# Kernel tuning notes

Hardware: AMD Instinct MI355X
Metric: run time of the kernel (lower is better)

Reference implementation:

```python
import jax, jax.numpy as jnp
import numpy as np

NEG_INF = jnp.float32(-1e9)  # finite large-negative avoids -inf*0 NaNs in grads


def setup_inputs() -> dict:
    key = jax.random.key(0)
    k1, k2, k3, k4, k5 = jax.random.split(key, 5)
    B, T, S, D = 16, 1024, 2048, 1024
    source = jax.random.normal(k1, (B, T, D), dtype=jnp.float32)
    memory_bank = jax.random.normal(k2, (B, S, D), dtype=jnp.float32)
    memory_lengths = jax.random.randint(k3, (B,), 1, S + 1, dtype=jnp.int32)
    # torch nn.Linear weights are [out_features, in_features]
    W_in = jax.random.normal(k4, (D, D), dtype=jnp.float32) / jnp.sqrt(jnp.float32(D))
    W_out = jax.random.normal(k5, (D, 2 * D), dtype=jnp.float32) / jnp.sqrt(jnp.float32(2 * D))
    return {"source": source, "memory_bank": memory_bank,
            "memory_lengths": memory_lengths, "W_in": W_in, "W_out": W_out}


def reference(source, memory_bank, memory_lengths, W_in, W_out):
    # GlobalAttention(attn_type='general', attn_func='softmax'), multi-step path
    B, T, D = source.shape
    S = memory_bank.shape[1]
    # score: general -> linear_in(h_t) @ h_s^T
    h_t = jnp.einsum('btd,ed->bte', source, W_in)            # [B,T,D]
    align = jnp.einsum('bte,bse->bts', h_t, memory_bank)      # [B,T,S]
    # sequence_mask on memory_lengths, broadcast over target dim
    mask = jnp.arange(S, dtype=jnp.int32)[None, None, :] < memory_lengths[:, None, None]
    align = jnp.where(mask, align, NEG_INF)
    align_vectors = jax.nn.softmax(align, axis=-1)            # [B,T,S]
    c = jnp.einsum('bts,bsd->btd', align_vectors, memory_bank)  # [B,T,D]
    concat_c = jnp.concatenate([c, source], axis=-1)          # [B,T,2D]
    attn_h = jnp.einsum('btf,of->bto', concat_c, W_out)       # linear_out, no bias for 'general'
    attn_h = jnp.tanh(attn_h)
    # not one_step -> transpose to [T,B,*]
    return attn_h.transpose(1, 0, 2), align_vectors.transpose(1, 0, 2)
```

## Files before the change

kernel.cpp:

```cpp
#include <hip/hip_runtime.h>

typedef __attribute__((ext_vector_type(8))) short s16x8;
typedef __attribute__((ext_vector_type(4))) float f32x4;
typedef __attribute__((ext_vector_type(4))) unsigned short u16x4;
typedef unsigned short u16;

__device__ __forceinline__ u16 f2bf(float x) {
  unsigned u = __builtin_bit_cast(unsigned, x);
  u = u + 0x7fffu + ((u >> 16) & 1u);
  return (u16)(u >> 16);
}
__device__ __forceinline__ float bf2f(u16 h) {
  return __builtin_bit_cast(float, (unsigned)h << 16);
}
__device__ __forceinline__ void split_bf(float x, u16 &h, u16 &l) {
  h = f2bf(x); l = f2bf(x - bf2f(h));
}

typedef __attribute__((address_space(1))) const unsigned int as1c_u32;
typedef __attribute__((address_space(3))) unsigned int as3_u32;
__device__ __forceinline__ void gload16(const void* g, void* l) {
  __builtin_amdgcn_global_load_lds((as1c_u32*)g, (as3_u32*)l, 16, 0, 0);
}

__global__ __launch_bounds__(256) void split_copy_k(
    const float* __restrict__ in, u16* __restrict__ oh, u16* __restrict__ ol, long n4) {
  const long i = (long)blockIdx.x * 256 + threadIdx.x;
  if (i >= n4) return;
  const f32x4 v = *(const f32x4*)(in + i * 4);
  u16x4 h, l;
#pragma unroll
  for (int e = 0; e < 4; ++e) { u16 hh, ll; split_bf(v[e], hh, ll); h[e] = hh; l[e] = ll; }
  *(u16x4*)(oh + i * 4) = h;
  *(u16x4*)(ol + i * 4) = l;
}

__global__ __launch_bounds__(256) void split_hi_k(
    const float* __restrict__ in, u16* __restrict__ oh, long n4) {
  const long i = (long)blockIdx.x * 256 + threadIdx.x;
  if (i >= n4) return;
  const f32x4 v = *(const f32x4*)(in + i * 4);
  u16x4 h;
#pragma unroll
  for (int e = 0; e < 4; ++e) h[e] = f2bf(v[e]);
  *(u16x4*)(oh + i * 4) = h;
}

__global__ __launch_bounds__(256) void transpose_bf_k(
    const u16* __restrict__ in, u16* __restrict__ outT) {
  __shared__ u16 tile[64][72];
  const int b = blockIdx.z;
  const int s0 = blockIdx.x * 64, d0 = blockIdx.y * 64;
  const u16* pin = in + (long)b * 2048 * 1024;
  u16* pout = outT + (long)b * 1024 * 2048;
  const int t = threadIdx.x;
#pragma unroll
  for (int i = 0; i < 4; ++i) {
    const int idx = i * 256 + t;
    const int r = idx >> 4;
    const int c4 = (idx & 15) * 4;
    *(u16x4*)&tile[r][c4] = *(const u16x4*)&pin[(long)(s0 + r) * 1024 + d0 + c4];
  }
  __syncthreads();
#pragma unroll
  for (int i = 0; i < 4; ++i) {
    const int idx = i * 256 + t;
    const int r = idx >> 4;
    const int c4 = (idx & 15) * 4;
    u16x4 v = { tile[c4][r], tile[c4 + 1][r], tile[c4 + 2][r], tile[c4 + 3][r] };
    *(u16x4*)&pout[(long)(d0 + r) * 2048 + s0 + c4] = v;
  }
}

__global__ __launch_bounds__(256) void softmax_k(
    float* __restrict__ alignBuf, const int* __restrict__ lens, float* __restrict__ outP) {
  const int row = blockIdx.x;
  const int b = row >> 10;
  const int tt = row & 1023;
  const int len = lens[b];
  float* arow = alignBuf + (long)row * 2048;
  const int t = threadIdx.x;
  const int lane = t & 63, wv = t >> 6;
  float v[8];
  float mx = -3.0e38f;
#pragma unroll
  for (int j = 0; j < 8; ++j) {
    const int s = j * 256 + t;
    float x = arow[s];
    x = (s < len) ? x : -1.0e9f;
    v[j] = x;
    mx = fmaxf(mx, x);
  }
#pragma unroll
  for (int off = 32; off; off >>= 1) mx = fmaxf(mx, __shfl_xor(mx, off));
  __shared__ float redm[4], reds[4];
  if (lane == 0) redm[wv] = mx;
  __syncthreads();
  mx = fmaxf(fmaxf(redm[0], redm[1]), fmaxf(redm[2], redm[3]));
  float e[8]; float sum = 0.f;
#pragma unroll
  for (int j = 0; j < 8; ++j) { e[j] = __expf(v[j] - mx); sum += e[j]; }
#pragma unroll
  for (int off = 32; off; off >>= 1) sum += __shfl_xor(sum, off);
  if (lane == 0) reds[wv] = sum;
  __syncthreads();
  sum = reds[0] + reds[1] + reds[2] + reds[3];
  const float inv = 1.0f / sum;
  u16* ph = (u16*)arow;
  u16* pl = ph + 2048;
  float* orow = outP + ((long)tt * 16 + b) * 2048;
#pragma unroll
  for (int j = 0; j < 8; ++j) {
    const int s = j * 256 + t;
    const float pv = e[j] * inv;
    orow[s] = pv;
    u16 h, l; split_bf(pv, h, l);
    ph[s] = h; pl[s] = l;
  }
}

template<int NPROD, int EP, int MASK>
__global__ __launch_bounds__(512, 2) void gemm256(
    const u16* __restrict__ Ah, const u16* __restrict__ Al,
    const u16* __restrict__ Ah2, const u16* __restrict__ Al2,
    int kSplitA, int lda, long sA,
    const u16* __restrict__ Bh, const u16* __restrict__ Bl, int ldb, long sB,
    int K, const int* __restrict__ lens,
    float* __restrict__ Cf, u16* __restrict__ Ch, u16* __restrict__ Cl,
    int ldc, long sC, int lgx, int lgxy, int nwg) {
  constexpr int NT = (NPROD >= 3) ? 4 : (NPROD == 2 ? 3 : 2);
  __shared__ __align__(16) u16 lds0[NT][8192];
  __shared__ __align__(16) u16 lds1[NT][8192];

  const int orig = blockIdx.x;
  const int wg = (orig & 7) * (nwg >> 3) + (orig >> 3);
  const int bx = wg & ((1 << lgx) - 1);
  const int by = (wg >> lgx) & ((1 << (lgxy - lgx)) - 1);
  const int bz = wg >> lgxy;

  const long m0 = (long)by * 256;
  const long n0 = (long)bx * 256;

  int Klim = K;
  if constexpr (MASK == 1) {
    const int len = lens[bz];
    if (n0 >= len) return;
  } else if constexpr (MASK == 2) {
    const int len = lens[bz];
    const int kl = (len + 31) & ~31;
    Klim = kl < K ? kl : K;
  }

  const u16* pAh  = Ah  + (long)bz * sA;
  const u16* pAl  = Al  + (long)bz * sA;
  const u16* pAh2 = Ah2 + (long)bz * sA;
  const u16* pAl2 = Al2 + (long)bz * sA;
  const u16* pBh  = Bh  + (long)bz * sB;
  const u16* pBl  = Bl  + (long)bz * sB;

  const int t = threadIdx.x;
  const int lane = t & 63;
  const int wv = t >> 6;
  const int wm = wv >> 2;
  const int wn = wv & 3;
  const int lk = lane >> 4;
  const int lr = lane & 15;

  f32x4 acc[8][4];
#pragma unroll
  for (int i = 0; i < 8; ++i)
#pragma unroll
    for (int j = 0; j < 4; ++j) acc[i][j] = 0.0f;

  auto stage = [&](u16 (*L)[8192], int k0) {
#pragma unroll
    for (int j = 0; j < 2; ++j) {
      const int ci = (j * 8 + wv) * 64;
      const int c = ci + lane;
      const int kc = c >> 8;
      const int r = c & 255;
      const int k = k0 + kc * 8;
      const u16 *aH = pAh, *aL = pAl;
      long ka = k;
      if (k >= kSplitA) { aH = pAh2; aL = pAl2; ka = k - kSplitA; }
      const long aoff = (m0 + r) * (long)lda + ka;
      gload16(aH + aoff, &L[0][ci * 8]);
      if constexpr (NPROD >= 2) gload16(aL + aoff, &L[2][ci * 8]);
      const long boff = (n0 + r) * (long)ldb + k;
      gload16(pBh + boff, &L[1][ci * 8]);
      if constexpr (NPROD >= 3) gload16(pBl + boff, &L[3][ci * 8]);
    }
  };

  auto compute = [&](u16 (*L)[8192]) {
    s16x8 bh[4], bl[4];
#pragma unroll
    for (int fn = 0; fn < 4; ++fn) {
      const int rb = wn * 64 + fn * 16 + lr;
      bh[fn] = *(const s16x8*)&L[1][lk * 2048 + rb * 8];
      if constexpr (NPROD >= 3) bl[fn] = *(const s16x8*)&L[3][lk * 2048 + rb * 8];
    }
#pragma unroll
    for (int fm = 0; fm < 8; ++fm) {
      const int ra = wm * 128 + fm * 16 + lr;
      const s16x8 ah = *(const s16x8*)&L[0][lk * 2048 + ra * 8];
      s16x8 al;
      if constexpr (NPROD >= 2) al = *(const s16x8*)&L[2][lk * 2048 + ra * 8];
#pragma unroll
      for (int fn = 0; fn < 4; ++fn) {
        acc[fm][fn] = __builtin_amdgcn_mfma_f32_16x16x32_bf16(ah, bh[fn], acc[fm][fn], 0, 0, 0);
        if constexpr (NPROD >= 3)
          acc[fm][fn] = __builtin_amdgcn_mfma_f32_16x16x32_bf16(ah, bl[fn], acc[fm][fn], 0, 0, 0);
        if constexpr (NPROD >= 2)
          acc[fm][fn] = __builtin_amdgcn_mfma_f32_16x16x32_bf16(al, bh[fn], acc[fm][fn], 0, 0, 0);
      }
    }
  };

  const int KT = Klim >> 5;
  stage(lds0, 0);
  __syncthreads();
  for (int kt = 0; kt < KT; kt += 2) {
    if (kt + 1 < KT) stage(lds1, (kt + 1) << 5);
    compute(lds0);
    __syncthreads();
    if (kt + 1 < KT) {
      if (kt + 2 < KT) stage(lds0, (kt + 2) << 5);
      compute(lds1);
      __syncthreads();
    }
  }

#pragma unroll
  for (int fm = 0; fm < 8; ++fm)
#pragma unroll
    for (int fn = 0; fn < 4; ++fn)
#pragma unroll
      for (int r = 0; r < 4; ++r) {
        const long row = m0 + wm * 128 + fm * 16 + (lane >> 4) * 4 + r;
        const long col = n0 + wn * 64 + fn * 16 + lr;
        const float v = acc[fm][fn][r];
        if constexpr (EP == 0) {
          Cf[(long)bz * sC + row * ldc + col] = v;
        } else if constexpr (EP == 1) {
          u16 h, l; split_bf(v, h, l);
          const long o = (long)bz * sC + row * ldc + col;
          Ch[o] = h; Cl[o] = l;
        } else {
          const long bb = row >> 10;
          const long tt = row & 1023;
          Cf[(tt * 16 + bb) * (long)ldc + col] = tanhf(v);
        }
      }
}

extern "C" void kernel_launch(void* const* d_in, const int* in_sizes, int n_in,
                              void* d_out, int out_size, void* d_ws, size_t ws_size,
                              hipStream_t stream) {
  (void)in_sizes; (void)n_in; (void)out_size; (void)ws_size;
  const float* src = (const float*)d_in[0];
  const float* mb  = (const float*)d_in[1];
  const int*   lens= (const int*)d_in[2];
  const float* Wi  = (const float*)d_in[3];
  const float* Wo  = (const float*)d_in[4];
  float* out = (float*)d_out;

  char* p = (char*)d_ws;
  u16* mbS_hi  = (u16*)p;
  u16* mbS_lo  = (u16*)(p + (64L << 20));
  u16* srcU_hi = (u16*)(p + (128L << 20));
  u16* srcU_lo = (u16*)(p + (160L << 20));
  u16* htc_hi  = (u16*)(p + (192L << 20));
  u16* htc_lo  = (u16*)(p + (224L << 20));
  float* alignBuf = (float*)(p + (256L << 20));
  u16* Wi_hi = (u16*)alignBuf;
  u16* Wi_lo = Wi_hi + 1048576;
  u16* mbT   = mbS_lo;
  u16* Wo_hi = mbS_hi;

  dim3 blk(256);
  split_copy_k<<<dim3(32768), blk, 0, stream>>>(mb,  mbS_hi, mbS_lo, 8388608L);
  split_copy_k<<<dim3(16384), blk, 0, stream>>>(src, srcU_hi, srcU_lo, 4194304L);
  split_copy_k<<<dim3(1024),  blk, 0, stream>>>(Wi,  Wi_hi,  Wi_lo,  262144L);

  gemm256<3, 1, 0><<<dim3(256), dim3(512), 0, stream>>>(
      srcU_hi, srcU_lo, srcU_hi, srcU_lo, 1 << 30, 1024, 0L,
      Wi_hi, Wi_lo, 1024, 0L,
      1024, lens,
      nullptr, htc_hi, htc_lo, 1024, 0L,
      2, 8, 256);

  gemm256<3, 0, 1><<<dim3(512), dim3(512), 0, stream>>>(
      htc_hi, htc_lo, htc_hi, htc_lo, 1 << 30, 1024, 1048576L,
      mbS_hi, mbS_lo, 1024, 2097152L,
      1024, lens,
      alignBuf, nullptr, nullptr, 2048, 2097152L,
      3, 5, 512);

  softmax_k<<<dim3(16384), blk, 0, stream>>>(alignBuf, lens, out + 16777216L);

  transpose_bf_k<<<dim3(32, 16, 16), blk, 0, stream>>>(mbS_hi, mbT);
  split_hi_k<<<dim3(2048), blk, 0, stream>>>(Wo, Wo_hi, 524288L);

  gemm256<2, 1, 2><<<dim3(256), dim3(512), 0, stream>>>(
      (const u16*)alignBuf, (const u16*)alignBuf + 2048,
      (const u16*)alignBuf, (const u16*)alignBuf + 2048, 1 << 30, 4096, 4194304L,
      mbT, mbT, 2048, 2097152L,
      2048, lens,
      nullptr, htc_hi, htc_lo, 1024, 1048576L,
      2, 4, 256);

  gemm256<2, 2, 0><<<dim3(256), dim3(512), 0, stream>>>(
      htc_hi, htc_lo, srcU_hi, srcU_lo, 1024, 1024, 0L,
      Wo_hi, Wo_hi, 2048, 0L,
      2048, lens,
      out, nullptr, nullptr, 1024, 0L,
      2, 8, 256);
}
```

Before: 975.7 us.

## Shrink GEMM tiles to 128x128 with 256 threads and single-buffered LDS

Replaces the 256x256-tile, 512-thread double-buffered GEMM with a 128x128-tile, 256-thread kernel that uses one LDS buffer and syncs twice per K step. Launch grids grow fourfold to cover the same outputs. The goal is more workgroups and occupancy across the CUs. In exchange it gives up operand reuse per tile and the overlap of global loads with MFMA compute that double buffering provided.

```diff
diff --git a/kernel.cpp b/kernel.cpp
--- a/kernel.cpp
+++ b/kernel.cpp
@@ -120,7 +120,7 @@
 }
 
 template<int NPROD, int EP, int MASK>
-__global__ __launch_bounds__(512, 2) void gemm256(
+__global__ __launch_bounds__(256) void gemm128(
     const u16* __restrict__ Ah, const u16* __restrict__ Al,
     const u16* __restrict__ Ah2, const u16* __restrict__ Al2,
     int kSplitA, int lda, long sA,
@@ -129,8 +129,7 @@
     float* __restrict__ Cf, u16* __restrict__ Ch, u16* __restrict__ Cl,
     int ldc, long sC, int lgx, int lgxy, int nwg) {
   constexpr int NT = (NPROD >= 3) ? 4 : (NPROD == 2 ? 3 : 2);
-  __shared__ __align__(16) u16 lds0[NT][8192];
-  __shared__ __align__(16) u16 lds1[NT][8192];
+  __shared__ __align__(16) u16 lds[NT][4096];
 
   const int orig = blockIdx.x;
   const int wg = (orig & 7) * (nwg >> 3) + (orig >> 3);
@@ -138,16 +137,14 @@
   const int by = (wg >> lgx) & ((1 << (lgxy - lgx)) - 1);
   const int bz = wg >> lgxy;
 
-  const long m0 = (long)by * 256;
-  const long n0 = (long)bx * 256;
+  const long m0 = (long)by * 128;
+  const long n0 = (long)bx * 128;
 
   int Klim = K;
   if constexpr (MASK == 1) {
-    const int len = lens[bz];
-    if (n0 >= len) return;
+    if (n0 >= lens[bz]) return;
   } else if constexpr (MASK == 2) {
-    const int len = lens[bz];
-    const int kl = (len + 31) & ~31;
+    const int kl = (lens[bz] + 31) & ~31;
     Klim = kl < K ? kl : K;
   }
 
@@ -161,83 +158,67 @@
   const int t = threadIdx.x;
   const int lane = t & 63;
   const int wv = t >> 6;
-  const int wm = wv >> 2;
-  const int wn = wv & 3;
+  const int wm = wv >> 1;
+  const int wn = wv & 1;
   const int lk = lane >> 4;
   const int lr = lane & 15;
 
-  f32x4 acc[8][4];
-#pragma unroll
-  for (int i = 0; i < 8; ++i)
+  f32x4 acc[4][4];
+#pragma unroll
+  for (int i = 0; i < 4; ++i)
 #pragma unroll
     for (int j = 0; j < 4; ++j) acc[i][j] = 0.0f;
 
-  auto stage = [&](u16 (*L)[8192], int k0) {
+  for (int k0 = 0; k0 < Klim; k0 += 32) {
+    __syncthreads();
 #pragma unroll
     for (int j = 0; j < 2; ++j) {
-      const int ci = (j * 8 + wv) * 64;
+      const int ci = (j * 4 + wv) * 64;
       const int c = ci + lane;
-      const int kc = c >> 8;
-      const int r = c & 255;
+      const int kc = c >> 7;
+      const int r = c & 127;
       const int k = k0 + kc * 8;
       const u16 *aH = pAh, *aL = pAl;
       long ka = k;
       if (k >= kSplitA) { aH = pAh2; aL = pAl2; ka = k - kSplitA; }
       const long aoff = (m0 + r) * (long)lda + ka;
-      gload16(aH + aoff, &L[0][ci * 8]);
-      if constexpr (NPROD >= 2) gload16(aL + aoff, &L[2][ci * 8]);
+      gload16(aH + aoff, &lds[0][ci * 8]);
+      if constexpr (NPROD >= 2) gload16(aL + aoff, &lds[2][ci * 8]);
       const long boff = (n0 + r) * (long)ldb + k;
-      gload16(pBh + boff, &L[1][ci * 8]);
-      if constexpr (NPROD >= 3) gload16(pBl + boff, &L[3][ci * 8]);
+      gload16(pBh + boff, &lds[1][ci * 8]);
+      if constexpr (NPROD >= 3) gload16(pBl + boff, &lds[3][ci * 8]);
     }
-  };
-
-  auto compute = [&](u16 (*L)[8192]) {
-    s16x8 bh[4], bl[4];
-#pragma unroll
-    for (int fn = 0; fn < 4; ++fn) {
-      const int rb = wn * 64 + fn * 16 + lr;
-      bh[fn] = *(const s16x8*)&L[1][lk * 2048 + rb * 8];
-      if constexpr (NPROD >= 3) bl[fn] = *(const s16x8*)&L[3][lk * 2048 + rb * 8];
+    __syncthreads();
+
+    s16x8 ah[4], al[4], bh[4], bl[4];
+#pragma unroll
+    for (int f = 0; f < 4; ++f) {
+      const int ra = wm * 64 + f * 16 + lr;
+      const int rb = wn * 64 + f * 16 + lr;
+      ah[f] = *(const s16x8*)&lds[0][lk * 1024 + ra * 8];
+      bh[f] = *(const s16x8*)&lds[1][lk * 1024 + rb * 8];
+      if constexpr (NPROD >= 2) al[f] = *(const s16x8*)&lds[2][lk * 1024 + ra * 8];
+      if constexpr (NPROD >= 3) bl[f] = *(const s16x8*)&lds[3][lk * 1024 + rb * 8];
     }
 #pragma unroll
-    for (int fm = 0; fm < 8; ++fm) {
-      const int ra = wm * 128 + fm * 16 + lr;
-      const s16x8 ah = *(const s16x8*)&L[0][lk * 2048 + ra * 8];
-      s16x8 al;
-      if constexpr (NPROD >= 2) al = *(const s16x8*)&L[2][lk * 2048 + ra * 8];
-#pragma unroll
-      for (int fn = 0; fn < 4; ++fn) {
-        acc[fm][fn] = __builtin_amdgcn_mfma_f32_16x16x32_bf16(ah, bh[fn], acc[fm][fn], 0, 0, 0);
+    for (int i = 0; i < 4; ++i)
+#pragma unroll
+      for (int j = 0; j < 4; ++j) {
+        acc[i][j] = __builtin_amdgcn_mfma_f32_16x16x32_bf16(ah[i], bh[j], acc[i][j], 0, 0, 0);
         if constexpr (NPROD >= 3)
-          acc[fm][fn] = __builtin_amdgcn_mfma_f32_16x16x32_bf16(ah, bl[fn], acc[fm][fn], 0, 0, 0);
+          acc[i][j] = __builtin_amdgcn_mfma_f32_16x16x32_bf16(ah[i], bl[j], acc[i][j], 0, 0, 0);
         if constexpr (NPROD >= 2)
-          acc[fm][fn] = __builtin_amdgcn_mfma_f32_16x16x32_bf16(al, bh[fn], acc[fm][fn], 0, 0, 0);
+          acc[i][j] = __builtin_amdgcn_mfma_f32_16x16x32_bf16(al[i], bh[j], acc[i][j], 0, 0, 0);
       }
-    }
-  };
-
-  const int KT = Klim >> 5;
-  stage(lds0, 0);
-  __syncthreads();
-  for (int kt = 0; kt < KT; kt += 2) {
-    if (kt + 1 < KT) stage(lds1, (kt + 1) << 5);
-    compute(lds0);
-    __syncthreads();
-    if (kt + 1 < KT) {
-      if (kt + 2 < KT) stage(lds0, (kt + 2) << 5);
-      compute(lds1);
-      __syncthreads();
-    }
-  }
-
-#pragma unroll
-  for (int fm = 0; fm < 8; ++fm)
+  }
+
+#pragma unroll
+  for (int fm = 0; fm < 4; ++fm)
 #pragma unroll
     for (int fn = 0; fn < 4; ++fn)
 #pragma unroll
       for (int r = 0; r < 4; ++r) {
-        const long row = m0 + wm * 128 + fm * 16 + (lane >> 4) * 4 + r;
+        const long row = m0 + wm * 64 + fm * 16 + (lane >> 4) * 4 + r;
         const long col = n0 + wn * 64 + fn * 16 + lr;
         const float v = acc[fm][fn][r];
         if constexpr (EP == 0) {
@@ -283,37 +264,37 @@
   split_copy_k<<<dim3(16384), blk, 0, stream>>>(src, srcU_hi, srcU_lo, 4194304L);
   split_copy_k<<<dim3(1024),  blk, 0, stream>>>(Wi,  Wi_hi,  Wi_lo,  262144L);
 
-  gemm256<3, 1, 0><<<dim3(256), dim3(512), 0, stream>>>(
+  gemm128<3, 1, 0><<<dim3(1024), blk, 0, stream>>>(
       srcU_hi, srcU_lo, srcU_hi, srcU_lo, 1 << 30, 1024, 0L,
       Wi_hi, Wi_lo, 1024, 0L,
       1024, lens,
       nullptr, htc_hi, htc_lo, 1024, 0L,
-      2, 8, 256);
-
-  gemm256<3, 0, 1><<<dim3(512), dim3(512), 0, stream>>>(
+      3, 10, 1024);
+
+  gemm128<3, 0, 1><<<dim3(2048), blk, 0, stream>>>(
       htc_hi, htc_lo, htc_hi, htc_lo, 1 << 30, 1024, 1048576L,
       mbS_hi, mbS_lo, 1024, 2097152L,
       1024, lens,
       alignBuf, nullptr, nullptr, 2048, 2097152L,
-      3, 5, 512);
+      4, 7, 2048);
 
   softmax_k<<<dim3(16384), blk, 0, stream>>>(alignBuf, lens, out + 16777216L);
 
   transpose_bf_k<<<dim3(32, 16, 16), blk, 0, stream>>>(mbS_hi, mbT);
   split_hi_k<<<dim3(2048), blk, 0, stream>>>(Wo, Wo_hi, 524288L);
 
-  gemm256<2, 1, 2><<<dim3(256), dim3(512), 0, stream>>>(
+  gemm128<2, 1, 2><<<dim3(1024), blk, 0, stream>>>(
       (const u16*)alignBuf, (const u16*)alignBuf + 2048,
       (const u16*)alignBuf, (const u16*)alignBuf + 2048, 1 << 30, 4096, 4194304L,
       mbT, mbT, 2048, 2097152L,
       2048, lens,
       nullptr, htc_hi, htc_lo, 1024, 1048576L,
-      2, 4, 256);
-
-  gemm256<2, 2, 0><<<dim3(256), dim3(512), 0, stream>>>(
+      3, 6, 1024);
+
+  gemm128<2, 2, 0><<<dim3(1024), blk, 0, stream>>>(
       htc_hi, htc_lo, srcU_hi, srcU_lo, 1024, 1024, 0L,
       Wo_hi, Wo_hi, 2048, 0L,
       2048, lens,
       out, nullptr, nullptr, 1024, 0L,
-      2, 8, 256);
-}
+      3, 10, 1024);
+}
```

After: 969.4 us. About the same (-0.6%).
